# Kernel tuning notes

Hardware: AMD Instinct MI355X
Metric: run time of the kernel (lower is better)

The kernel has to match this reference:

```python
import jax, jax.numpy as jnp
import numpy as np


def _interp_linear_align_corners(w, new_len):
    """Linear (bilinear with trivial 2nd axis) interpolation along last axis,
    align_corners=True, matching torch F.interpolate. w: (..., k) -> (..., new_len)."""
    k = w.shape[-1]
    scale = (k - 1) / (new_len - 1) if new_len > 1 else 0.0
    pos = jnp.arange(new_len, dtype=w.dtype) * jnp.asarray(scale, w.dtype)
    lo = jnp.floor(pos).astype(jnp.int32)
    hi = jnp.minimum(lo + 1, k - 1)
    frac = pos - lo.astype(w.dtype)
    return w[..., lo] * (1.0 - frac) + w[..., hi] * frac


def _depthwise_conv(x, kernel, pad_h, pad_w):
    # x: (B,C,H,W), kernel: (C,1,Kh,Kw), groups=C
    C = x.shape[1]
    return jax.lax.conv_general_dilated(
        x, kernel, window_strides=(1, 1),
        padding=[(pad_h, pad_h), (pad_w, pad_w)],
        dimension_numbers=("NCHW", "OIHW", "NCHW"),
        feature_group_count=C)


def setup_inputs() -> dict:
    key = jax.random.key(0)
    k1, k2, k3, k4, k5 = jax.random.split(key, 5)
    dim, ksize = 128, 13
    B, H, W = 32, 64, 64
    fan = 1.0 / np.sqrt(ksize)  # torch Conv2d default init scale (groups=dim -> fan_in=k)
    return {
        "x": jax.random.normal(k1, (B, dim, H, W), dtype=jnp.float32),
        "h_weight": jax.random.uniform(k2, (dim, 1, ksize, 1), jnp.float32, -fan, fan),
        "w_weight": jax.random.uniform(k3, (dim, 1, 1, ksize), jnp.float32, -fan, fan),
        "h_bias": jax.random.uniform(k4, (dim,), jnp.float32, -fan, fan),
        "w_bias": jax.random.uniform(k5, (dim,), jnp.float32, -fan, fan),
    }


def reference(x, h_weight, w_weight, h_bias, w_bias):
    B, C, H, W = x.shape
    Kh, Kw = 2 * H - 1, 2 * W - 1
    # Interpolate base kernels to instance kernel sizes (align_corners=True bilinear,
    # degenerate to 1-D linear since the other spatial dim has size 1).
    hk = _interp_linear_align_corners(h_weight[:, :, :, 0], Kh)[..., None]   # (C,1,Kh,1)
    wk = _interp_linear_align_corners(w_weight[:, :, 0, :], Kw)[:, :, None]  # (C,1,1,Kw)
    y = _depthwise_conv(x, hk, H - 1, 0) + h_bias[None, :, None, None]
    y = _depthwise_conv(y, wk, 0, W - 1) + w_bias[None, :, None, None]
    return y
```

## Files before the change

### kernel.cpp

```cpp
#include <hip/hip_runtime.h>


#define STRB 72
#define MSTR 120

typedef short  bfrag  __attribute__((ext_vector_type(8)));
typedef float  f32x4  __attribute__((ext_vector_type(4)));
typedef unsigned short us4 __attribute__((ext_vector_type(4)));

__device__ __forceinline__ unsigned short f2bf(float f) {
    unsigned u = __builtin_bit_cast(unsigned, f);
    u += 0x7fffu + ((u >> 16) & 1u);
    return (unsigned short)(u >> 16);
}
__device__ __forceinline__ float bf2f(unsigned short h) {
    unsigned u = ((unsigned)h) << 16;
    return __builtin_bit_cast(float, u);
}

__device__ __forceinline__ void lds_barrier() {
    asm volatile("s_waitcnt lgkmcnt(0)" ::: "memory");
    __builtin_amdgcn_s_barrier();
}

__global__ __launch_bounds__(256, 6)
void oversize_conv_v7(const float* __restrict__ x,
                      const float* __restrict__ hwt,
                      const float* __restrict__ wwt,
                      const float* __restrict__ hb,
                      const float* __restrict__ wb,
                      float* __restrict__ out)
{
    __shared__ __align__(16) unsigned short Xs[64 * STRB];
    __shared__ __align__(16) unsigned short PT[64 * STRB];
    __shared__ __align__(16) unsigned short Mw[16 * MSTR];
    __shared__ __align__(16) unsigned short Mh[16 * MSTR];
    __shared__ unsigned short hkb[128], wkb[128];
    __shared__ __align__(16) float sw[64];

    const int tid = threadIdx.x;
    const int c    = blockIdx.x & 127;
    const int pair = blockIdx.x >> 7;
    const size_t imgStride = (size_t)128 * 4096;
    const size_t img0 = ((size_t)(2 * pair) * 128 + c) * 4096;

    const int wv = tid >> 6, lane = tid & 63;
    const int r = lane & 15, gq = lane >> 4;

    float4 xv[4];
    {
        const float4* xg = (const float4*)(x + img0);
        #pragma unroll
        for (int q = 0; q < 4; ++q) xv[q] = xg[tid + q * 256];
    }

    if (tid < 127) {
        const float scale = 12.0f / 126.0f;
        float pos = (float)tid * scale;
        int   lo  = (int)pos;
        float fr  = pos - (float)lo;
        int   hi  = (lo + 1 < 12) ? lo + 1 : 12;
        hkb[tid] = f2bf(hwt[c * 13 + lo] * (1.0f - fr) + hwt[c * 13 + hi] * fr);
        wkb[tid] = f2bf(wwt[c * 13 + lo] * (1.0f - fr) + wwt[c * 13 + hi] * fr);
    }
    lds_barrier();

    for (int k = tid; k < 16 * 112; k += 256) {
        int rr  = k / 112;
        int col = k - rr * 112;
        int t   = col + 15 - rr;
        Mw[rr * MSTR + col] = wkb[t];
        Mh[rr * MSTR + col] = hkb[t];
    }
    if (tid < 64) {
        float s = 0.f;
        #pragma unroll 8
        for (int iw = 0; iw < 64; ++iw) s += bf2f(wkb[iw - tid + 63]);
        sw[tid] = s;
    }
    #pragma unroll
    for (int q = 0; q < 4; ++q) {
        int idx = tid + q * 256;
        int row = idx >> 4;
        int col = (idx & 15) * 4;
        us4 v;
        v[0] = f2bf(xv[q].x); v[1] = f2bf(xv[q].y);
        v[2] = f2bf(xv[q].z); v[3] = f2bf(xv[q].w);
        *(us4*)&Xs[row * STRB + col] = v;
    }
    float4 xn[4];
    {
        const float4* xg = (const float4*)(x + img0 + imgStride);
        #pragma unroll
        for (int q = 0; q < 4; ++q) xn[q] = xg[tid + q * 256];
    }
    lds_barrier();

    const float hbc = hb[c], wbc = wb[c];
    f32x4 sw4 = *(const f32x4*)&sw[16 * wv + 4 * gq];
    f32x4 bias;
    bias[0] = hbc * sw4[0] + wbc; bias[1] = hbc * sw4[1] + wbc;
    bias[2] = hbc * sw4[2] + wbc; bias[3] = hbc * sw4[3] + wbc;

    #pragma unroll
    for (int i = 0; i < 2; ++i) {
        bfrag a0 = *(const bfrag*)&Xs[(16 * wv + r) * STRB + 8 * gq];
        bfrag a1 = *(const bfrag*)&Xs[(16 * wv + r) * STRB + 32 + 8 * gq];
        f32x4 acc[4] = {};
        #pragma unroll
        for (int nt = 0; nt < 4; ++nt) {
            const int mb = r * MSTR + 8 * gq - 16 * nt + 48;
            bfrag b0 = *(const bfrag*)&Mw[mb];
            bfrag b1 = *(const bfrag*)&Mw[mb + 32];
            acc[nt] = __builtin_amdgcn_mfma_f32_16x16x32_bf16(a0, b0, acc[nt], 0, 0, 0);
            acc[nt] = __builtin_amdgcn_mfma_f32_16x16x32_bf16(a1, b1, acc[nt], 0, 0, 0);
        }
        #pragma unroll
        for (int nt = 0; nt < 4; ++nt) {
            us4 p;
            p[0] = f2bf(acc[nt][0]); p[1] = f2bf(acc[nt][1]);
            p[2] = f2bf(acc[nt][2]); p[3] = f2bf(acc[nt][3]);
            *(us4*)&PT[(16 * nt + r) * STRB + 16 * wv + 4 * gq] = p;
        }
        lds_barrier();

        bfrag pa0 = *(const bfrag*)&PT[(16 * wv + r) * STRB + 8 * gq];
        bfrag pa1 = *(const bfrag*)&PT[(16 * wv + r) * STRB + 32 + 8 * gq];
        f32x4 acc2[4] = {bias, bias, bias, bias};
        #pragma unroll
        for (int nt = 0; nt < 4; ++nt) {
            const int mb = r * MSTR + 8 * gq - 16 * nt + 48;
            bfrag bh0 = *(const bfrag*)&Mh[mb];
            bfrag bh1 = *(const bfrag*)&Mh[mb + 32];
            acc2[nt] = __builtin_amdgcn_mfma_f32_16x16x32_bf16(pa0, bh0, acc2[nt], 0, 0, 0);
            acc2[nt] = __builtin_amdgcn_mfma_f32_16x16x32_bf16(pa1, bh1, acc2[nt], 0, 0, 0);
        }

        if (i == 0) {
            #pragma unroll
            for (int q = 0; q < 4; ++q) {
                int idx = tid + q * 256;
                int row = idx >> 4;
                int col = (idx & 15) * 4;
                us4 v;
                v[0] = f2bf(xn[q].x); v[1] = f2bf(xn[q].y);
                v[2] = f2bf(xn[q].z); v[3] = f2bf(xn[q].w);
                *(us4*)&Xs[row * STRB + col] = v;
            }
        }

        {
            float* og = out + img0 + (size_t)i * imgStride;
            #pragma unroll
            for (int nt = 0; nt < 4; ++nt) {
                f32x4 v = acc2[nt];
                *(f32x4*)&og[(size_t)(16 * nt + r) * 64 + 16 * wv + 4 * gq] = v;
            }
        }

        lds_barrier();
    }
}

extern "C" void kernel_launch(void* const* d_in, const int* in_sizes, int n_in,
                              void* d_out, int out_size, void* d_ws, size_t ws_size,
                              hipStream_t stream)
{
    const float* x   = (const float*)d_in[0];
    const float* hwt = (const float*)d_in[1];
    const float* wwt = (const float*)d_in[2];
    const float* hb  = (const float*)d_in[3];
    const float* wb  = (const float*)d_in[4];
    oversize_conv_v7<<<2048, 256, 0, stream>>>(x, hwt, wwt, hb, wb, (float*)d_out);
}
```

Baseline: 27.24 us.

## Process four images per block with double-buffered input and wave-local W pass

Each block now handles four images of one channel instead of two, halving the grid and reusing the per-channel Toeplitz matrices across more images. The input tile is double-buffered in LDS and the next image is prefetched from global memory while the current one is computed. The W-pass MFMA is restructured so each wave produces its own rows of the intermediate, with its Toeplitz B fragment hoisted into registers, which removes the barrier between the two passes. The costs are more LDS, lower launch-bounds occupancy and fewer blocks in flight.

```diff
diff --git a/kernel.cpp b/kernel.cpp
--- a/kernel.cpp
+++ b/kernel.cpp
@@ -23,15 +23,15 @@
     __builtin_amdgcn_s_barrier();
 }
 
-__global__ __launch_bounds__(256, 6)
-void oversize_conv_v7(const float* __restrict__ x,
+__global__ __launch_bounds__(256, 4)
+void oversize_conv_v8(const float* __restrict__ x,
                       const float* __restrict__ hwt,
                       const float* __restrict__ wwt,
                       const float* __restrict__ hb,
                       const float* __restrict__ wb,
                       float* __restrict__ out)
 {
-    __shared__ __align__(16) unsigned short Xs[64 * STRB];
+    __shared__ __align__(16) unsigned short Xs[2][64 * STRB];
     __shared__ __align__(16) unsigned short PT[64 * STRB];
     __shared__ __align__(16) unsigned short Mw[16 * MSTR];
     __shared__ __align__(16) unsigned short Mh[16 * MSTR];
@@ -39,10 +39,10 @@
     __shared__ __align__(16) float sw[64];
 
     const int tid = threadIdx.x;
-    const int c    = blockIdx.x & 127;
-    const int pair = blockIdx.x >> 7;
+    const int c   = blockIdx.x & 127;
+    const int g4  = blockIdx.x >> 7;
     const size_t imgStride = (size_t)128 * 4096;
-    const size_t img0 = ((size_t)(2 * pair) * 128 + c) * 4096;
+    const size_t img0 = ((size_t)(4 * g4) * 128 + c) * 4096;
 
     const int wv = tid >> 6, lane = tid & 63;
     const int r = lane & 15, gq = lane >> 4;
@@ -86,7 +86,7 @@
         us4 v;
         v[0] = f2bf(xv[q].x); v[1] = f2bf(xv[q].y);
         v[2] = f2bf(xv[q].z); v[3] = f2bf(xv[q].w);
-        *(us4*)&Xs[row * STRB + col] = v;
+        *(us4*)&Xs[0][row * STRB + col] = v;
     }
     float4 xn[4];
     {
@@ -96,6 +96,10 @@
     }
     lds_barrier();
 
+    const int mbase = r * MSTR + 8 * gq + 48;
+    bfrag bW0 = *(const bfrag*)&Mw[mbase - 16 * wv];
+    bfrag bW1 = *(const bfrag*)&Mw[mbase - 16 * wv + 32];
+
     const float hbc = hb[c], wbc = wb[c];
     f32x4 sw4 = *(const f32x4*)&sw[16 * wv + 4 * gq];
     f32x4 bias;
@@ -103,40 +107,38 @@
     bias[2] = hbc * sw4[2] + wbc; bias[3] = hbc * sw4[3] + wbc;
 
     #pragma unroll
-    for (int i = 0; i < 2; ++i) {
-        bfrag a0 = *(const bfrag*)&Xs[(16 * wv + r) * STRB + 8 * gq];
-        bfrag a1 = *(const bfrag*)&Xs[(16 * wv + r) * STRB + 32 + 8 * gq];
-        f32x4 acc[4] = {};
+    for (int i = 0; i < 4; ++i) {
+        const unsigned short* xb = Xs[i & 1];
+
+        f32x4 accA[4] = {};
         #pragma unroll
-        for (int nt = 0; nt < 4; ++nt) {
-            const int mb = r * MSTR + 8 * gq - 16 * nt + 48;
-            bfrag b0 = *(const bfrag*)&Mw[mb];
-            bfrag b1 = *(const bfrag*)&Mw[mb + 32];
-            acc[nt] = __builtin_amdgcn_mfma_f32_16x16x32_bf16(a0, b0, acc[nt], 0, 0, 0);
-            acc[nt] = __builtin_amdgcn_mfma_f32_16x16x32_bf16(a1, b1, acc[nt], 0, 0, 0);
+        for (int m = 0; m < 4; ++m) {
+            bfrag a0 = *(const bfrag*)&xb[(16 * m + r) * STRB + 8 * gq];
+            bfrag a1 = *(const bfrag*)&xb[(16 * m + r) * STRB + 32 + 8 * gq];
+            accA[m] = __builtin_amdgcn_mfma_f32_16x16x32_bf16(a0, bW0, accA[m], 0, 0, 0);
+            accA[m] = __builtin_amdgcn_mfma_f32_16x16x32_bf16(a1, bW1, accA[m], 0, 0, 0);
         }
         #pragma unroll
-        for (int nt = 0; nt < 4; ++nt) {
+        for (int m = 0; m < 4; ++m) {
             us4 p;
-            p[0] = f2bf(acc[nt][0]); p[1] = f2bf(acc[nt][1]);
-            p[2] = f2bf(acc[nt][2]); p[3] = f2bf(acc[nt][3]);
-            *(us4*)&PT[(16 * nt + r) * STRB + 16 * wv + 4 * gq] = p;
+            p[0] = f2bf(accA[m][0]); p[1] = f2bf(accA[m][1]);
+            p[2] = f2bf(accA[m][2]); p[3] = f2bf(accA[m][3]);
+            *(us4*)&PT[(16 * wv + r) * STRB + 16 * m + 4 * gq] = p;
         }
-        lds_barrier();
 
         bfrag pa0 = *(const bfrag*)&PT[(16 * wv + r) * STRB + 8 * gq];
         bfrag pa1 = *(const bfrag*)&PT[(16 * wv + r) * STRB + 32 + 8 * gq];
         f32x4 acc2[4] = {bias, bias, bias, bias};
         #pragma unroll
         for (int nt = 0; nt < 4; ++nt) {
-            const int mb = r * MSTR + 8 * gq - 16 * nt + 48;
-            bfrag bh0 = *(const bfrag*)&Mh[mb];
-            bfrag bh1 = *(const bfrag*)&Mh[mb + 32];
+            bfrag bh0 = *(const bfrag*)&Mh[mbase - 16 * nt];
+            bfrag bh1 = *(const bfrag*)&Mh[mbase - 16 * nt + 32];
             acc2[nt] = __builtin_amdgcn_mfma_f32_16x16x32_bf16(pa0, bh0, acc2[nt], 0, 0, 0);
             acc2[nt] = __builtin_amdgcn_mfma_f32_16x16x32_bf16(pa1, bh1, acc2[nt], 0, 0, 0);
         }
 
-        if (i == 0) {
+        if (i < 3) {
+            unsigned short* xalt = (unsigned short*)Xs[(i + 1) & 1];
             #pragma unroll
             for (int q = 0; q < 4; ++q) {
                 int idx = tid + q * 256;
@@ -145,8 +147,13 @@
                 us4 v;
                 v[0] = f2bf(xn[q].x); v[1] = f2bf(xn[q].y);
                 v[2] = f2bf(xn[q].z); v[3] = f2bf(xn[q].w);
-                *(us4*)&Xs[row * STRB + col] = v;
+                *(us4*)&xalt[row * STRB + col] = v;
             }
+        }
+        if (i < 2) {
+            const float4* xg = (const float4*)(x + img0 + (size_t)(i + 2) * imgStride);
+            #pragma unroll
+            for (int q = 0; q < 4; ++q) xn[q] = xg[tid + q * 256];
         }
 
         {
@@ -171,5 +178,5 @@
     const float* wwt = (const float*)d_in[2];
     const float* hb  = (const float*)d_in[3];
     const float* wb  = (const float*)d_in[4];
-    oversize_conv_v7<<<2048, 256, 0, stream>>>(x, hwt, wwt, hb, wb, (float*)d_out);
+    oversize_conv_v8<<<1024, 256, 0, stream>>>(x, hwt, wwt, hb, wb, (float*)d_out);
 }
```

Measured after the change: 25.45 us. -6.6%, faster.
